# Optimization experiments

Measured on AMD Instinct MI355X. Metric: run time of the kernel, lower is better.

The kernel has to match this reference:

```python
import jax, jax.numpy as jnp
import numpy as np

R = 256            # rois_per_image = cfg.TRAIN.BATCH_SIZE
FG_QUOTA = 64      # round(FG_FRACTION=0.25 * R)
FG_THRESH = 0.5
BG_HI = 0.5
BG_LO = 0.0
MEANS = jnp.array([0.0, 0.0, 0.0, 0.0], jnp.float32)
STDS = jnp.array([0.1, 0.1, 0.2, 0.2], jnp.float32)
INSIDE_W = jnp.array([1.0, 1.0, 1.0, 1.0], jnp.float32)


def _iou(boxes, gt):
    # boxes [B,M,4], gt [B,G,4] -> IoU [B,M,G]  (bbox_overlaps_batch2)
    x1 = jnp.maximum(boxes[:, :, None, 0], gt[:, None, :, 0])
    y1 = jnp.maximum(boxes[:, :, None, 1], gt[:, None, :, 1])
    x2 = jnp.minimum(boxes[:, :, None, 2], gt[:, None, :, 2])
    y2 = jnp.minimum(boxes[:, :, None, 3], gt[:, None, :, 3])
    iw = jnp.clip(x2 - x1 + 1.0, 0.0)
    ih = jnp.clip(y2 - y1 + 1.0, 0.0)
    inter = iw * ih
    area_b = (boxes[..., 2] - boxes[..., 0] + 1.0) * (boxes[..., 3] - boxes[..., 1] + 1.0)
    area_g = (gt[..., 2] - gt[..., 0] + 1.0) * (gt[..., 3] - gt[..., 1] + 1.0)
    return inter / (area_b[:, :, None] + area_g[:, None, :] - inter)


def _bbox_transform(ex, gt):
    # bbox_transform_batch2: ex,gt [B,R,4] -> targets [B,R,4]
    ew = ex[..., 2] - ex[..., 0] + 1.0
    eh = ex[..., 3] - ex[..., 1] + 1.0
    ecx = ex[..., 0] + 0.5 * ew
    ecy = ex[..., 1] + 0.5 * eh
    gw = gt[..., 2] - gt[..., 0] + 1.0
    gh = gt[..., 3] - gt[..., 1] + 1.0
    gcx = gt[..., 0] + 0.5 * gw
    gcy = gt[..., 1] + 0.5 * gh
    return jnp.stack([(gcx - ecx) / ew, (gcy - ecy) / eh,
                      jnp.log(gw / ew), jnp.log(gh / eh)], axis=-1)


def setup_inputs() -> dict:
    key = jax.random.key(0)
    B, N, G, IMG = 16, 12000, 128, 800.0
    ks = jax.random.split(key, 8)

    def boxes(k1, k2, n):
        xy = jax.random.uniform(k1, (B, n, 2)) * (IMG - 260.0)
        wh = 16.0 + jax.random.uniform(k2, (B, n, 2)) * 240.0
        return jnp.concatenate([xy, xy + wh], axis=-1)

    roi_xy = boxes(ks[0], ks[1], N)
    bidx = jnp.broadcast_to(jnp.arange(B, dtype=jnp.float32)[:, None, None], (B, N, 1))
    all_rois = jnp.concatenate([bidx, roi_xy], axis=-1)  # [B,N,5]

    gt_xy = boxes(ks[2], ks[3], G)
    gt_lab = jax.random.randint(ks[4], (B, G, 1), 1, 151).astype(jnp.float32)
    gt_boxes = jnp.concatenate([gt_xy, gt_lab], axis=-1)  # [B,G,5]
    return {"all_rois": all_rois, "gt_boxes": gt_boxes}


def reference(all_rois, gt_boxes):
    B, N, _ = all_rois.shape
    G = gt_boxes.shape[1]
    bidx = jnp.arange(B, dtype=all_rois.dtype)

    # append gt boxes as extra proposals (first col = image index)
    gt_append = jnp.concatenate(
        [jnp.broadcast_to(bidx[:, None, None], (B, G, 1)), gt_boxes[:, :, :4]], axis=2)
    rois_all = jnp.concatenate([all_rois, gt_append], axis=1)  # [B,M,5], M=N+G

    ov = _iou(rois_all[..., 1:5], gt_boxes[..., :4])  # [B,M,G]
    max_ov = ov.max(axis=2)
    gt_asgn = ov.argmax(axis=2)
    labels = jnp.take_along_axis(gt_boxes[..., 4], gt_asgn, axis=1)  # [B,M]

    fg_mask = max_ov >= FG_THRESH
    bg_mask = (max_ov < BG_HI) & (max_ov >= BG_LO)

    # deterministic random sampling via keyed top_k (replaces np.random.permutation)
    k1, k2 = jax.random.split(jax.random.key(42))
    r1 = jax.random.uniform(k1, max_ov.shape)
    r2 = jax.random.uniform(k2, max_ov.shape)
    _, fg_top = jax.lax.top_k(jnp.where(fg_mask, r1 + 2.0, r1), R)  # fg first, randomized
    _, bg_top = jax.lax.top_k(jnp.where(bg_mask, r2 + 2.0, r2), R)

    fg_num = fg_mask.sum(axis=1)
    bg_num = bg_mask.sum(axis=1)
    fg_count = jnp.minimum(fg_num, FG_QUOTA)[:, None]          # [B,1]
    bg_avail = jnp.clip(bg_num, 1, R)[:, None]
    pos = jnp.broadcast_to(jnp.arange(R)[None, :], (B, R))

    fg_pick = jnp.take_along_axis(fg_top, jnp.minimum(pos, jnp.maximum(fg_count - 1, 0)), axis=1)
    bg_pick = jnp.take_along_axis(bg_top, (pos - fg_count) % bg_avail, axis=1)
    keep = jnp.where(pos < fg_count, fg_pick, bg_pick)         # [B,R]

    lab = jnp.take_along_axis(labels, keep, axis=1)
    lab = jnp.where(pos < fg_count, lab, 0.0)                  # bg -> class 0

    rois = jnp.take_along_axis(rois_all, keep[..., None], axis=1)  # [B,R,5]
    rois = rois.at[..., 0].set(bidx[:, None])

    asgn = jnp.take_along_axis(gt_asgn, keep, axis=1)
    gt_sel = jnp.take_along_axis(gt_boxes[..., :4], asgn[..., None], axis=1)

    t = (_bbox_transform(rois[..., 1:5], gt_sel) - MEANS) / STDS
    fg4 = (lab > 0).astype(t.dtype)[..., None]
    bbox_targets = t * fg4
    inside_w = fg4 * INSIDE_W
    outside_w = (inside_w > 0).astype(t.dtype)
    return rois, lab, bbox_targets, inside_w, outside_w
```

## Files before the change

kernel.cpp:

```cpp
#include <hip/hip_runtime.h>
#include <cstdint>
#include <cstddef>


#define THREEFRY_PARTITIONABLE 1

constexpr int kB = 16;
constexpr int kN = 12000;
constexpr int kG = 128;
constexpr int kM = kN + kG;
constexpr int kM4 = kM / 4;
constexpr int kR = 256;
constexpr int kFgQuota = 64;
constexpr unsigned kSeedHi = 0u;
constexpr unsigned kSeedLo = 42u;

__device__ __forceinline__ int imin(int a, int b) { return a < b ? a : b; }
__device__ __forceinline__ int imax(int a, int b) { return a > b ? a : b; }

__device__ __forceinline__ unsigned rotl32(unsigned v, int d) {
  return (v << d) | (v >> (32 - d));
}

__device__ __forceinline__ void tf2x32(unsigned k0, unsigned k1,
                                       unsigned x0, unsigned x1,
                                       unsigned& o0, unsigned& o1) {
  const unsigned k2 = k0 ^ k1 ^ 0x1BD11BDAu;
  x0 += k0; x1 += k1;
#define TF_R(d) x0 += x1; x1 = rotl32(x1, d); x1 ^= x0;
  TF_R(13) TF_R(15) TF_R(26) TF_R(6)
  x0 += k1; x1 += k2 + 1u;
  TF_R(17) TF_R(29) TF_R(16) TF_R(24)
  x0 += k2; x1 += k0 + 2u;
  TF_R(13) TF_R(15) TF_R(26) TF_R(6)
  x0 += k0; x1 += k1 + 3u;
  TF_R(17) TF_R(29) TF_R(16) TF_R(24)
  x0 += k1; x1 += k2 + 4u;
  TF_R(13) TF_R(15) TF_R(26) TF_R(6)
  x0 += k2; x1 += k0 + 5u;
#undef TF_R
  o0 = x0; o1 = x1;
}

__device__ __forceinline__ void derive_key(int which, unsigned& ka, unsigned& kb) {
#if THREEFRY_PARTITIONABLE
  tf2x32(kSeedHi, kSeedLo, 0u, (unsigned)which, ka, kb);
#else
  unsigned a0, a1, b0, b1;
  tf2x32(kSeedHi, kSeedLo, 0u, 2u, a0, a1);
  tf2x32(kSeedHi, kSeedLo, 1u, 3u, b0, b1);
  if (which == 0) { ka = a0; kb = b0; } else { ka = a1; kb = b1; }
#endif
}

__device__ __forceinline__ float bits_to_uniform(unsigned bits) {
  return __uint_as_float((bits >> 9) | 0x3f800000u) - 1.0f;
}

__device__ __forceinline__ float jax_uniform(unsigned ka, unsigned kb, unsigned i) {
#if THREEFRY_PARTITIONABLE
  unsigned o0, o1;
  tf2x32(ka, kb, 0u, i, o0, o1);
  return bits_to_uniform(o0 ^ o1);
#else
  const unsigned H = (unsigned)(kB * kM) / 2u;
  unsigned o0, o1;
  if (i < H) { tf2x32(ka, kb, i, i + H, o0, o1); return bits_to_uniform(o0); }
  else       { tf2x32(ka, kb, i - H, i, o0, o1); return bits_to_uniform(o1); }
#endif
}

__global__ __launch_bounds__(256) void k_prep(const float* __restrict__ all_rois,
                                              const float* __restrict__ gt_boxes,
                                              int* __restrict__ asgn,
                                              unsigned* __restrict__ vb) {
  __shared__ float4 sg[kG];
  __shared__ float sga[kG];
  const int b = blockIdx.y;
  const int m = blockIdx.x * 256 + threadIdx.x;
  if (threadIdx.x < kG) {
    const float* gp = gt_boxes + ((size_t)b * kG + threadIdx.x) * 5;
    const float x0 = gp[0], y0 = gp[1], x1 = gp[2], y1 = gp[3];
    sg[threadIdx.x] = make_float4(x0, y0, x1, y1);
    sga[threadIdx.x] = ((x1 - x0) + 1.0f) * ((y1 - y0) + 1.0f);
  }
  __syncthreads();
  if (m >= kM) return;

  float bx0, by0, bx1, by1;
  if (m < kN) {
    const float* rp = all_rois + ((size_t)b * kN + m) * 5;
    bx0 = rp[1]; by0 = rp[2]; bx1 = rp[3]; by1 = rp[4];
  } else {
    const float4 g4 = sg[m - kN];
    bx0 = g4.x; by0 = g4.y; bx1 = g4.z; by1 = g4.w;
  }
  const float areab = ((bx1 - bx0) + 1.0f) * ((by1 - by0) + 1.0f);

  float best = -1.0f;
  int bi = 0;
  for (int g = 0; g < kG; ++g) {
    const float4 g4 = sg[g];
    const float xx0 = fmaxf(bx0, g4.x);
    const float yy0 = fmaxf(by0, g4.y);
    const float xx1 = fminf(bx1, g4.z);
    const float yy1 = fminf(by1, g4.w);
    const float iw = fmaxf((xx1 - xx0) + 1.0f, 0.0f);
    const float ih = fmaxf((yy1 - yy0) + 1.0f, 0.0f);
    const float inter = iw * ih;
    const float iou = inter / ((areab + sga[g]) - inter);
    if (iou > best) { best = iou; bi = g; }
  }
  asgn[(size_t)b * kM + m] = bi;

  unsigned k1a, k1b, k2a, k2b;
  derive_key(0, k1a, k1b);
  derive_key(1, k2a, k2b);
  const unsigned i = (unsigned)(b * kM + m);
  const float r1 = jax_uniform(k1a, k1b, i);
  const float r2 = jax_uniform(k2a, k2b, i);
  const bool fg = best >= 0.5f;
  const bool bg = (best < 0.5f) && (best >= 0.0f);
  const float v1 = fg ? (r1 + 2.0f) : r1;
  const float v2 = bg ? (r2 + 2.0f) : r2;
  vb[(size_t)b * kM + m] = __float_as_uint(v1);
  vb[(size_t)(kB + b) * kM + m] = __float_as_uint(v2);
}

__device__ __forceinline__ int block_reduce_sum(int v, int* s_red, int tid) {
#pragma unroll
  for (int off = 32; off > 0; off >>= 1) v += __shfl_down(v, off, 64);
  __syncthreads();
  if ((tid & 63) == 0) s_red[tid >> 6] = v;
  __syncthreads();
  return s_red[0] + s_red[1] + s_red[2] + s_red[3];
}

__device__ __forceinline__ unsigned mask_bin(unsigned v) {
  unsigned bn = (v - 0x40000000u) >> 11;
  return bn > 2047u ? 2047u : bn;
}

__global__ __launch_bounds__(256) void k_select(const unsigned* __restrict__ vb,
                                                int* __restrict__ topidx,
                                                int* __restrict__ nin) {
  __shared__ uint4 s_vb4[kM4];
  __shared__ int s_hist[2048];
  __shared__ unsigned long long s_cand[1024];
  __shared__ int s_scan[256];
  __shared__ int s_red[4];
  __shared__ unsigned long long s_wmax[4];
  __shared__ int s_tbin, s_cnt;
  unsigned* s_vb = (unsigned*)s_vb4;

  const int which = blockIdx.x;
  const int b = blockIdx.y;
  const int tid = threadIdx.x;
  const unsigned* src = vb + (size_t)(which * kB + b) * kM;
  int* dst = topidx + (size_t)(which * kB + b) * kR;

  for (int i = tid; i < 2048; i += 256) s_hist[i] = 0;
  if (tid == 0) s_cnt = 0;
  __syncthreads();

  int local = 0;
  for (int i = tid; i < kM4; i += 256) {
    const uint4 u = ((const uint4*)src)[i];
    s_vb4[i] = u;
#define HBIN(x) if ((x) >= 0x40000000u) { ++local; atomicAdd(&s_hist[mask_bin(x)], 1); }
    HBIN(u.x) HBIN(u.y) HBIN(u.z) HBIN(u.w)
#undef HBIN
  }
  const int n_in = block_reduce_sum(local, s_red, tid);
  if (tid == 0) nin[which * kB + b] = n_in;
  const int quota = (which == 0) ? kFgQuota : kR;
  const int K = imin(n_in, quota);
  __syncthreads();

  if (K == 0) {
    if (which == 0) return;
    unsigned long long best = 0ull;
    for (int m = tid; m < kM; m += 256) {
      const unsigned long long key =
          ((unsigned long long)s_vb[m] << 32) | (unsigned)(0xFFFFFFFFu - (unsigned)m);
      if (key > best) best = key;
    }
#pragma unroll
    for (int off = 32; off > 0; off >>= 1) {
      const unsigned long long o = __shfl_down(best, off, 64);
      if (o > best) best = o;
    }
    if ((tid & 63) == 0) s_wmax[tid >> 6] = best;
    __syncthreads();
    if (tid == 0) {
      for (int w = 1; w < 4; ++w) if (s_wmax[w] > best) best = s_wmax[w];
      dst[0] = (int)(0xFFFFFFFFu - (unsigned)(best & 0xFFFFFFFFull));
    }
    return;
  }

  const int base = 2048 - 8 * (tid + 1);
  int s = 0;
#pragma unroll
  for (int j = 0; j < 8; ++j) s += s_hist[base + j];
  s_scan[tid] = s;
  __syncthreads();
  for (int off = 1; off < 256; off <<= 1) {
    const int add = (tid >= off) ? s_scan[tid - off] : 0;
    __syncthreads();
    s_scan[tid] += add;
    __syncthreads();
  }
  const int above = s_scan[tid] - s;
  int cum = above;
  for (int j = 7; j >= 0; --j) {
    const int c = s_hist[base + j];
    if (cum < K && cum + c >= K) s_tbin = base + j;
    cum += c;
  }
  __syncthreads();
  const unsigned tbin = (unsigned)s_tbin;

  for (int m = tid; m < kM; m += 256) {
    const unsigned v = s_vb[m];
    if (v >= 0x40000000u && mask_bin(v) >= tbin) {
      const int p = atomicAdd(&s_cnt, 1);
      if (p < 1024)
        s_cand[p] = ((unsigned long long)v << 32) | (unsigned)(0xFFFFFFFFu - (unsigned)m);
    }
  }
  __syncthreads();
  const int Nc = imin(s_cnt, 1024);

  for (int j = tid; j < Nc; j += 256) {
    const unsigned long long key = s_cand[j];
    int rank = 0;
    for (int i = 0; i < Nc; ++i) rank += (s_cand[i] > key) ? 1 : 0;
    if (rank < K)
      dst[rank] = (int)(0xFFFFFFFFu - (unsigned)(key & 0xFFFFFFFFull));
  }
}

__global__ __launch_bounds__(256) void k_finalize(const float* __restrict__ all_rois,
                                                  const float* __restrict__ gt_boxes,
                                                  const int* __restrict__ asgn,
                                                  const int* __restrict__ topidx,
                                                  const int* __restrict__ nin,
                                                  float* __restrict__ out) {
  const int b = blockIdx.x;
  const int pos = threadIdx.x;
  const int fgnum = nin[b];
  const int bgnum = nin[kB + b];
  const int fgc = imin(fgnum, kFgQuota);
  const int bgav = imin(imax(bgnum, 1), kR);
  const int* fgtop = topidx + (size_t)b * kR;
  const int* bgtop = topidx + (size_t)(kB + b) * kR;

  const bool isfg = pos < fgc;
  int keep;
  if (isfg) keep = fgtop[imin(pos, imax(fgc - 1, 0))];
  else      keep = bgtop[(pos - fgc) % bgav];

  float bx0, by0, bx1, by1;
  if (keep < kN) {
    const float* rp = all_rois + ((size_t)b * kN + keep) * 5;
    bx0 = rp[1]; by0 = rp[2]; bx1 = rp[3]; by1 = rp[4];
  } else {
    const float* gp = gt_boxes + ((size_t)b * kG + (keep - kN)) * 5;
    bx0 = gp[0]; by0 = gp[1]; bx1 = gp[2]; by1 = gp[3];
  }
  const int a = asgn[(size_t)b * kM + keep];
  const float* gp = gt_boxes + ((size_t)b * kG + a) * 5;
  const float gx0 = gp[0], gy0 = gp[1], gx1 = gp[2], gy1 = gp[3];
  const float lab = isfg ? gp[4] : 0.0f;
  const float fg4 = (lab > 0.0f) ? 1.0f : 0.0f;

  const float ew = (bx1 - bx0) + 1.0f;
  const float eh = (by1 - by0) + 1.0f;
  const float ecx = bx0 + 0.5f * ew;
  const float ecy = by0 + 0.5f * eh;
  const float gw = (gx1 - gx0) + 1.0f;
  const float gh = (gy1 - gy0) + 1.0f;
  const float gcx = gx0 + 0.5f * gw;
  const float gcy = gy0 + 0.5f * gh;
  const float t0 = ((gcx - ecx) / ew) / 0.1f;
  const float t1 = ((gcy - ecy) / eh) / 0.1f;
  const float t2 = logf(gw / ew) / 0.2f;
  const float t3 = logf(gh / eh) / 0.2f;

  float* o_rois = out;
  float* o_lab  = out + (size_t)kB * kR * 5;
  float* o_tgt  = o_lab + (size_t)kB * kR;
  float* o_iw   = o_tgt + (size_t)kB * kR * 4;
  float* o_ow   = o_iw  + (size_t)kB * kR * 4;
  const size_t p = (size_t)b * kR + pos;
  o_rois[p * 5 + 0] = (float)b;
  o_rois[p * 5 + 1] = bx0;
  o_rois[p * 5 + 2] = by0;
  o_rois[p * 5 + 3] = bx1;
  o_rois[p * 5 + 4] = by1;
  o_lab[p] = lab;
  o_tgt[p * 4 + 0] = t0 * fg4;
  o_tgt[p * 4 + 1] = t1 * fg4;
  o_tgt[p * 4 + 2] = t2 * fg4;
  o_tgt[p * 4 + 3] = t3 * fg4;
  o_iw[p * 4 + 0] = fg4; o_iw[p * 4 + 1] = fg4;
  o_iw[p * 4 + 2] = fg4; o_iw[p * 4 + 3] = fg4;
  o_ow[p * 4 + 0] = fg4; o_ow[p * 4 + 1] = fg4;
  o_ow[p * 4 + 2] = fg4; o_ow[p * 4 + 3] = fg4;
}

extern "C" void kernel_launch(void* const* d_in, const int* in_sizes, int n_in_args,
                              void* d_out, int out_size, void* d_ws, size_t ws_size,
                              hipStream_t stream) {
  (void)in_sizes; (void)n_in_args; (void)out_size; (void)ws_size;
  const float* all_rois = (const float*)d_in[0];
  const float* gt_boxes = (const float*)d_in[1];
  float* out = (float*)d_out;

  char* ws = (char*)d_ws;
  int* asgn    = (int*)ws;
  unsigned* vb = (unsigned*)(ws + (size_t)kB * kM * 4);
  int* nin     = (int*)(ws + (size_t)kB * kM * 4 * 3);
  int* topidx  = nin + 64;

  dim3 gA((kM + 255) / 256, kB);
  k_prep<<<gA, 256, 0, stream>>>(all_rois, gt_boxes, asgn, vb);
  dim3 gB(2, kB);
  k_select<<<gB, 256, 0, stream>>>(vb, topidx, nin);
  k_finalize<<<kB, kR, 0, stream>>>(all_rois, gt_boxes, asgn, topidx, nin, out);
}
```

Before: 104.8 us.

## Replace argmax IoU with division-free fg test and move histogram into prep

The prep kernel no longer computes a full argmax IoU or stores assignments. It only tests whether any gt gives IoU >= 0.5, using an fma comparison in place of a division, and builds the per-image selection histograms with global atomics. The select kernel reads the precomputed histogram and streams candidates straight from global memory instead of staging 48KB in LDS. The finalize kernel recomputes the argmax only for the 256 kept rois per image, at the cost of a memset and global atomic contention in prep.

Result: slower. 110.2 us (+5.1%).

```diff
diff --git a/kernel.cpp b/kernel.cpp
--- a/kernel.cpp
+++ b/kernel.cpp
@@ -70,10 +70,15 @@
 #endif
 }
 
+__device__ __forceinline__ unsigned mask_bin(unsigned v) {
+  unsigned bn = (v - 0x40000000u) >> 11;
+  return bn > 2047u ? 2047u : bn;
+}
+
 __global__ __launch_bounds__(256) void k_prep(const float* __restrict__ all_rois,
                                               const float* __restrict__ gt_boxes,
-                                              int* __restrict__ asgn,
-                                              unsigned* __restrict__ vb) {
+                                              unsigned* __restrict__ vb,
+                                              int* __restrict__ hist) {
   __shared__ float4 sg[kG];
   __shared__ float sga[kG];
   const int b = blockIdx.y;
@@ -97,8 +102,8 @@
   }
   const float areab = ((bx1 - bx0) + 1.0f) * ((by1 - by0) + 1.0f);
 
-  float best = -1.0f;
-  int bi = 0;
+  bool fg = false;
+#pragma unroll 8
   for (int g = 0; g < kG; ++g) {
     const float4 g4 = sg[g];
     const float xx0 = fmaxf(bx0, g4.x);
@@ -108,10 +113,9 @@
     const float iw = fmaxf((xx1 - xx0) + 1.0f, 0.0f);
     const float ih = fmaxf((yy1 - yy0) + 1.0f, 0.0f);
     const float inter = iw * ih;
-    const float iou = inter / ((areab + sga[g]) - inter);
-    if (iou > best) { best = iou; bi = g; }
-  }
-  asgn[(size_t)b * kM + m] = bi;
+    const float denom = (areab + sga[g]) - inter;
+    fg = fg || (__builtin_fmaf(-0.5f, denom, inter) >= (-0x1p-26f) * denom);
+  }
 
   unsigned k1a, k1b, k2a, k2b;
   derive_key(0, k1a, k1b);
@@ -119,12 +123,14 @@
   const unsigned i = (unsigned)(b * kM + m);
   const float r1 = jax_uniform(k1a, k1b, i);
   const float r2 = jax_uniform(k2a, k2b, i);
-  const bool fg = best >= 0.5f;
-  const bool bg = (best < 0.5f) && (best >= 0.0f);
   const float v1 = fg ? (r1 + 2.0f) : r1;
-  const float v2 = bg ? (r2 + 2.0f) : r2;
-  vb[(size_t)b * kM + m] = __float_as_uint(v1);
-  vb[(size_t)(kB + b) * kM + m] = __float_as_uint(v2);
+  const float v2 = fg ? r2 : (r2 + 2.0f);
+  const unsigned u1 = __float_as_uint(v1);
+  const unsigned u2 = __float_as_uint(v2);
+  vb[(size_t)b * kM + m] = u1;
+  vb[(size_t)(kB + b) * kM + m] = u2;
+  if (fg) atomicAdd(&hist[(size_t)b * 2048 + mask_bin(u1)], 1);
+  else    atomicAdd(&hist[(size_t)(kB + b) * 2048 + mask_bin(u2)], 1);
 }
 
 __device__ __forceinline__ int block_reduce_sum(int v, int* s_red, int tid) {
@@ -136,53 +142,43 @@
   return s_red[0] + s_red[1] + s_red[2] + s_red[3];
 }
 
-__device__ __forceinline__ unsigned mask_bin(unsigned v) {
-  unsigned bn = (v - 0x40000000u) >> 11;
-  return bn > 2047u ? 2047u : bn;
-}
-
 __global__ __launch_bounds__(256) void k_select(const unsigned* __restrict__ vb,
+                                                const int* __restrict__ hist,
                                                 int* __restrict__ topidx,
                                                 int* __restrict__ nin) {
-  __shared__ uint4 s_vb4[kM4];
   __shared__ int s_hist[2048];
   __shared__ unsigned long long s_cand[1024];
   __shared__ int s_scan[256];
   __shared__ int s_red[4];
   __shared__ unsigned long long s_wmax[4];
   __shared__ int s_tbin, s_cnt;
-  unsigned* s_vb = (unsigned*)s_vb4;
 
   const int which = blockIdx.x;
   const int b = blockIdx.y;
   const int tid = threadIdx.x;
   const unsigned* src = vb + (size_t)(which * kB + b) * kM;
+  const int* hrow = hist + (size_t)(which * kB + b) * 2048;
   int* dst = topidx + (size_t)(which * kB + b) * kR;
 
-  for (int i = tid; i < 2048; i += 256) s_hist[i] = 0;
+  for (int i = tid; i < 2048; i += 256) s_hist[i] = hrow[i];
   if (tid == 0) s_cnt = 0;
   __syncthreads();
 
-  int local = 0;
-  for (int i = tid; i < kM4; i += 256) {
-    const uint4 u = ((const uint4*)src)[i];
-    s_vb4[i] = u;
-#define HBIN(x) if ((x) >= 0x40000000u) { ++local; atomicAdd(&s_hist[mask_bin(x)], 1); }
-    HBIN(u.x) HBIN(u.y) HBIN(u.z) HBIN(u.w)
-#undef HBIN
-  }
-  const int n_in = block_reduce_sum(local, s_red, tid);
+  const int base = 2048 - 8 * (tid + 1);
+  int s = 0;
+#pragma unroll
+  for (int j = 0; j < 8; ++j) s += s_hist[base + j];
+  const int n_in = block_reduce_sum(s, s_red, tid);
   if (tid == 0) nin[which * kB + b] = n_in;
   const int quota = (which == 0) ? kFgQuota : kR;
   const int K = imin(n_in, quota);
-  __syncthreads();
 
   if (K == 0) {
     if (which == 0) return;
     unsigned long long best = 0ull;
     for (int m = tid; m < kM; m += 256) {
       const unsigned long long key =
-          ((unsigned long long)s_vb[m] << 32) | (unsigned)(0xFFFFFFFFu - (unsigned)m);
+          ((unsigned long long)src[m] << 32) | (unsigned)(0xFFFFFFFFu - (unsigned)m);
       if (key > best) best = key;
     }
 #pragma unroll
@@ -199,10 +195,6 @@
     return;
   }
 
-  const int base = 2048 - 8 * (tid + 1);
-  int s = 0;
-#pragma unroll
-  for (int j = 0; j < 8; ++j) s += s_hist[base + j];
   s_scan[tid] = s;
   __syncthreads();
   for (int off = 1; off < 256; off <<= 1) {
@@ -221,13 +213,18 @@
   __syncthreads();
   const unsigned tbin = (unsigned)s_tbin;
 
-  for (int m = tid; m < kM; m += 256) {
-    const unsigned v = s_vb[m];
-    if (v >= 0x40000000u && mask_bin(v) >= tbin) {
-      const int p = atomicAdd(&s_cnt, 1);
-      if (p < 1024)
-        s_cand[p] = ((unsigned long long)v << 32) | (unsigned)(0xFFFFFFFFu - (unsigned)m);
+  const uint4* src4 = (const uint4*)src;
+  for (int i = tid; i < kM4; i += 256) {
+    const uint4 u = src4[i];
+#define CAND(x, j)                                                         \
+    if ((x) >= 0x40000000u && mask_bin(x) >= tbin) {                       \
+      const int p = atomicAdd(&s_cnt, 1);                                  \
+      if (p < 1024)                                                        \
+        s_cand[p] = ((unsigned long long)(x) << 32) |                      \
+                    (unsigned)(0xFFFFFFFFu - (unsigned)(4 * i + (j)));     \
     }
+    CAND(u.x, 0) CAND(u.y, 1) CAND(u.z, 2) CAND(u.w, 3)
+#undef CAND
   }
   __syncthreads();
   const int Nc = imin(s_cnt, 1024);
@@ -241,14 +238,25 @@
   }
 }
 
-__global__ __launch_bounds__(256) void k_finalize(const float* __restrict__ all_rois,
-                                                  const float* __restrict__ gt_boxes,
-                                                  const int* __restrict__ asgn,
-                                                  const int* __restrict__ topidx,
-                                                  const int* __restrict__ nin,
-                                                  float* __restrict__ out) {
+__global__ __launch_bounds__(256) void k_final(const float* __restrict__ all_rois,
+                                               const float* __restrict__ gt_boxes,
+                                               const int* __restrict__ topidx,
+                                               const int* __restrict__ nin,
+                                               float* __restrict__ out) {
+  __shared__ float4 sg[kG];
+  __shared__ float sga[kG];
+  __shared__ float slab[kG];
   const int b = blockIdx.x;
   const int pos = threadIdx.x;
+  if (threadIdx.x < kG) {
+    const float* gp = gt_boxes + ((size_t)b * kG + threadIdx.x) * 5;
+    const float x0 = gp[0], y0 = gp[1], x1 = gp[2], y1 = gp[3];
+    sg[threadIdx.x] = make_float4(x0, y0, x1, y1);
+    sga[threadIdx.x] = ((x1 - x0) + 1.0f) * ((y1 - y0) + 1.0f);
+    slab[threadIdx.x] = gp[4];
+  }
+  __syncthreads();
+
   const int fgnum = nin[b];
   const int bgnum = nin[kB + b];
   const int fgc = imin(fgnum, kFgQuota);
@@ -266,13 +274,29 @@
     const float* rp = all_rois + ((size_t)b * kN + keep) * 5;
     bx0 = rp[1]; by0 = rp[2]; bx1 = rp[3]; by1 = rp[4];
   } else {
-    const float* gp = gt_boxes + ((size_t)b * kG + (keep - kN)) * 5;
-    bx0 = gp[0]; by0 = gp[1]; bx1 = gp[2]; by1 = gp[3];
-  }
-  const int a = asgn[(size_t)b * kM + keep];
-  const float* gp = gt_boxes + ((size_t)b * kG + a) * 5;
-  const float gx0 = gp[0], gy0 = gp[1], gx1 = gp[2], gy1 = gp[3];
-  const float lab = isfg ? gp[4] : 0.0f;
+    const float4 g4 = sg[keep - kN];
+    bx0 = g4.x; by0 = g4.y; bx1 = g4.z; by1 = g4.w;
+  }
+  const float areab = ((bx1 - bx0) + 1.0f) * ((by1 - by0) + 1.0f);
+
+  float best = -1.0f;
+  int a = 0;
+  for (int g = 0; g < kG; ++g) {
+    const float4 g4 = sg[g];
+    const float xx0 = fmaxf(bx0, g4.x);
+    const float yy0 = fmaxf(by0, g4.y);
+    const float xx1 = fminf(bx1, g4.z);
+    const float yy1 = fminf(by1, g4.w);
+    const float iw = fmaxf((xx1 - xx0) + 1.0f, 0.0f);
+    const float ih = fmaxf((yy1 - yy0) + 1.0f, 0.0f);
+    const float inter = iw * ih;
+    const float iou = inter / ((areab + sga[g]) - inter);
+    if (iou > best) { best = iou; a = g; }
+  }
+
+  const float4 gt4 = sg[a];
+  const float gx0 = gt4.x, gy0 = gt4.y, gx1 = gt4.z, gy1 = gt4.w;
+  const float lab = isfg ? slab[a] : 0.0f;
   const float fg4 = (lab > 0.0f) ? 1.0f : 0.0f;
 
   const float ew = (bx1 - bx0) + 1.0f;
@@ -319,14 +343,15 @@
   float* out = (float*)d_out;
 
   char* ws = (char*)d_ws;
-  int* asgn    = (int*)ws;
-  unsigned* vb = (unsigned*)(ws + (size_t)kB * kM * 4);
-  int* nin     = (int*)(ws + (size_t)kB * kM * 4 * 3);
-  int* topidx  = nin + 64;
-
+  unsigned* vb = (unsigned*)ws;
+  int* hist    = (int*)(ws + 1572864);
+  int* topidx  = (int*)(ws + 1572864 + 262144);
+  int* nin     = (int*)(ws + 1572864 + 262144 + 32768);
+
+  hipMemsetAsync(hist, 0, (size_t)2 * kB * 2048 * sizeof(int), stream);
   dim3 gA((kM + 255) / 256, kB);
-  k_prep<<<gA, 256, 0, stream>>>(all_rois, gt_boxes, asgn, vb);
+  k_prep<<<gA, 256, 0, stream>>>(all_rois, gt_boxes, vb, hist);
   dim3 gB(2, kB);
-  k_select<<<gB, 256, 0, stream>>>(vb, topidx, nin);
-  k_finalize<<<kB, kR, 0, stream>>>(all_rois, gt_boxes, asgn, topidx, nin, out);
-}
+  k_select<<<gB, 256, 0, stream>>>(vb, hist, topidx, nin);
+  k_final<<<kB, kR, 0, stream>>>(all_rois, gt_boxes, topidx, nin, out);
+}
```
